# Kernel optimization log

Hardware: AMD Instinct MI355X
Metric: run time of the kernel (lower is better)

Reference implementation:

```python
import jax, jax.numpy as jnp
import numpy as np

EMB = 1024
HEADS = 16
HEAD_DIM = EMB // HEADS


def setup_inputs() -> dict:
    key = jax.random.key(0)
    ks = jax.random.split(key, 12)
    B, S = 4, 2048
    s = 1.0 / np.sqrt(EMB)
    inp = {
        "query": jax.random.normal(ks[0], (B, S, EMB), jnp.float32),
        "key": jax.random.normal(ks[1], (B, S, EMB), jnp.float32),
        "value": jax.random.normal(ks[2], (B, S, EMB), jnp.float32),
        "mask": jax.random.randint(ks[3], (B, 1, 1, S), 0, 2) > 0,
        "Wq": jax.random.normal(ks[4], (EMB, EMB), jnp.float32) * s,
        "bq": jax.random.normal(ks[5], (EMB,), jnp.float32) * s,
        "Wk": jax.random.normal(ks[6], (EMB, EMB), jnp.float32) * s,
        "bk": jax.random.normal(ks[7], (EMB,), jnp.float32) * s,
        "Wv": jax.random.normal(ks[8], (EMB, EMB), jnp.float32) * s,
        "bv": jax.random.normal(ks[9], (EMB,), jnp.float32) * s,
        "Wo": jax.random.normal(ks[10], (EMB, EMB), jnp.float32) * s,
        "bo": jax.random.normal(ks[11], (EMB,), jnp.float32) * s,
    }
    return inp


def _split(x):
    # (B, S, E) -> (B, H, S, D)
    B, S, _ = x.shape
    return x.reshape(B, S, HEADS, HEAD_DIM).transpose(0, 2, 1, 3)


def reference(query, key, value, mask, Wq, bq, Wk, bk, Wv, bv, Wo, bo):
    q = _split(query @ Wq + bq)
    k = _split(key @ Wk + bk)
    v = _split(value @ Wv + bv)
    scale = 1.0 / np.sqrt(HEAD_DIM).astype(np.float32)
    # (B, H, S, S) score matrix, explicitly materialized as in the original
    scores = jnp.einsum("bhqd,bhkd->bhqk", q, k) * scale
    scores = jnp.where(mask, scores, -jnp.inf)
    probs = jax.nn.softmax(scores, axis=-1)
    attn = jnp.einsum("bhqk,bhkd->bhqd", probs, v)
    B, _, S, _ = attn.shape
    out = attn.transpose(0, 2, 1, 3).reshape(B, S, EMB)
    return out @ Wo + bo
```

## Files before the change

### kernel.cpp

```cpp
#include <hip/hip_runtime.h>
#include <hip/hip_bf16.h>
#include <stdint.h>

#define EMB 1024
#define HEADS 16
#define HDIM 64
#define BATCH 4
#define SEQ 2048
#define MTOT (BATCH * SEQ)

typedef unsigned short u16;
typedef __attribute__((ext_vector_type(8))) short bf16x8;
typedef __attribute__((ext_vector_type(4))) float f32x4;

__device__ inline u16 f2bf(float f) {
    uint32_t u = __builtin_bit_cast(uint32_t, f);
    u += 0x7fffu + ((u >> 16) & 1u);
    return (u16)(u >> 16);
}

__device__ inline uint32_t pk2bf(float a, float b) {
    uint32_t ua = __builtin_bit_cast(uint32_t, a) + 0x8000u;
    uint32_t ub = __builtin_bit_cast(uint32_t, b) + 0x8000u;
    return (ua >> 16) | (ub & 0xffff0000u);
}

__device__ inline f32x4 mfma16(bf16x8 a, bf16x8 b, f32x4 c) {
    return __builtin_amdgcn_mfma_f32_16x16x32_bf16(a, b, c, 0, 0, 0);
}

#define GLDS16(gp, lp)                                                        \
    __builtin_amdgcn_global_load_lds(                                         \
        (const __attribute__((address_space(1))) void*)(gp),                  \
        (__attribute__((address_space(3))) void*)(lp), 16, 0, 0)

__global__ void mask_compact(const int* __restrict__ mask,
                             int* __restrict__ cnt, int* __restrict__ idx) {
    __shared__ int ps[256];
    const int b = blockIdx.x, tid = threadIdx.x;
    const int* mp = mask + (size_t)b * SEQ;
    int m[8], s = 0;
#pragma unroll
    for (int e = 0; e < 8; ++e) {
        m[e] = mp[tid * 8 + e] ? 1 : 0;
        s += m[e];
    }
    ps[tid] = s;
    __syncthreads();
    for (int off = 1; off < 256; off <<= 1) {
        int v = (tid >= off) ? ps[tid - off] : 0;
        __syncthreads();
        if (tid >= off) ps[tid] += v;
        __syncthreads();
    }
    const int total = ps[255];
    int r = ps[tid] - s;
#pragma unroll
    for (int e = 0; e < 8; ++e)
        if (m[e]) idx[b * SEQ + r++] = tid * 8 + e;
    if (tid == 0) cnt[b] = total;
}

__global__ void gather_cast(const float* __restrict__ src,
                            const int* __restrict__ idx,
                            const int* __restrict__ cnt,
                            u16* __restrict__ dst) {
    const int row = blockIdx.x;
    const int b = row >> 11, j = row & (SEQ - 1);
    const int cn = cnt[b];
    const int cp = (cn + 127) & ~127;
    if (j >= cp) return;
    const int c4 = threadIdx.x;
    float4 v = {0.f, 0.f, 0.f, 0.f};
    if (j < cn) {
        const int srow = idx[b * SEQ + j];
        v = ((const float4*)(src + (size_t)(b * SEQ + srow) * EMB))[c4];
    }
    ushort4 o;
    o.x = f2bf(v.x); o.y = f2bf(v.y); o.z = f2bf(v.z); o.w = f2bf(v.w);
    ((ushort4*)(dst + (size_t)row * EMB))[c4] = o;
}

__global__ void cast_f32_bf16(const float* __restrict__ src,
                              u16* __restrict__ dst, int n4) {
    int i = blockIdx.x * blockDim.x + threadIdx.x;
    if (i >= n4) return;
    float4 v = ((const float4*)src)[i];
    ushort4 o;
    o.x = f2bf(v.x); o.y = f2bf(v.y); o.z = f2bf(v.z); o.w = f2bf(v.w);
    ((ushort4*)dst)[i] = o;
}

__global__ void transpose_cast(const float* __restrict__ W,
                               u16* __restrict__ Wt) {
    __shared__ u16 T[64][65];
    const int kb = blockIdx.y * 64, nb = blockIdx.x * 64;
    const int tr = threadIdx.x >> 4;
    const int tc = (threadIdx.x & 15) * 4;
#pragma unroll
    for (int j = 0; j < 4; ++j) {
        int r = tr + j * 16;
        float4 v = *(const float4*)&W[(size_t)(kb + r) * EMB + nb + tc];
        T[tc + 0][r] = f2bf(v.x);
        T[tc + 1][r] = f2bf(v.y);
        T[tc + 2][r] = f2bf(v.z);
        T[tc + 3][r] = f2bf(v.w);
    }
    __syncthreads();
#pragma unroll
    for (int j = 0; j < 4; ++j) {
        int rr = tr + j * 16;
        ushort4 o;
        o.x = T[rr][tc]; o.y = T[rr][tc + 1];
        o.z = T[rr][tc + 2]; o.w = T[rr][tc + 3];
        *(ushort4*)&Wt[(size_t)(nb + rr) * EMB + kb + tc] = o;
    }
}

__global__ void transpose_v(const u16* __restrict__ Vp, u16* __restrict__ Vt,
                            const int* __restrict__ cnt) {
    __shared__ u16 T[64][65];
    const int h = blockIdx.x;
    const int b = blockIdx.y >> 5;
    const int s0 = (blockIdx.y & 31) * 64;
    const int cp = (cnt[b] + 127) & ~127;
    if (s0 >= cp) return;
    const int tr = threadIdx.x >> 3;
    const int tc = (threadIdx.x & 7) * 8;
#pragma unroll
    for (int j = 0; j < 2; ++j) {
        int sr = tr + j * 32;
        uint4 v = *(const uint4*)&Vp[(size_t)(b * SEQ + s0 + sr) * EMB +
                                     h * 64 + tc];
        const u16* p = (const u16*)&v;
#pragma unroll
        for (int e = 0; e < 8; ++e) T[tc + e][sr] = p[e];
    }
    __syncthreads();
#pragma unroll
    for (int j = 0; j < 2; ++j) {
        int d = tr + j * 32;
        u16 tmp[8];
#pragma unroll
        for (int e = 0; e < 8; ++e) tmp[e] = T[d][tc + e];
        const int base32 = s0 + (tc & 32);
        const int p0 = ((tc & 8) << 1) + ((tc & 16) >> 2);
        const size_t rowoff =
            ((size_t)(b * HEADS + h) * HDIM + d) * SEQ;
        *(uint2*)&Vt[rowoff + base32 + p0] = *(const uint2*)&tmp[0];
        *(uint2*)&Vt[rowoff + base32 + p0 + 8] = *(const uint2*)&tmp[4];
    }
}

template <bool OUT_BF16>
__global__ __launch_bounds__(256, 2) void gemm_bt(
    const u16* __restrict__ A, const u16* __restrict__ Bt,
    const float* __restrict__ bias, void* __restrict__ C,
    int M, int N, int K, float scale, const int* __restrict__ cnt) {
    __shared__ __align__(16) u16 As[128 * 32];
    __shared__ __align__(16) u16 Bs[128 * 32];
    const int m0 = blockIdx.y * 128, n0 = blockIdx.x * 128;
    if (cnt) {
        const int bb = m0 >> 11;
        const int cp = (cnt[bb] + 127) & ~127;
        if ((m0 & (SEQ - 1)) >= cp) return;
    }
    const int tid = threadIdx.x;
    const int w = tid >> 6, l = tid & 63;
    const int quad = l >> 4, l16 = l & 15;
    const int wm = (w >> 1) * 64, wn = (w & 1) * 64;

    f32x4 acc[4][4];
#pragma unroll
    for (int i = 0; i < 4; ++i)
#pragma unroll
        for (int j = 0; j < 4; ++j) acc[i][j] = (f32x4){0.f, 0.f, 0.f, 0.f};

    for (int k0 = 0; k0 < K; k0 += 32) {
        __syncthreads();
#pragma unroll
        for (int i = 0; i < 2; ++i) {
            int c = (w * 2 + i) * 64 + l;
            int r = c >> 2;
            int sc = (c & 3) ^ ((r >> 1) & 3);
            GLDS16(A + (size_t)(m0 + r) * K + k0 + sc * 8, &As[c * 8]);
            GLDS16(Bt + (size_t)(n0 + r) * K + k0 + sc * 8, &Bs[c * 8]);
        }
        __syncthreads();
        bf16x8 af[4], bfr[4];
#pragma unroll
        for (int mt = 0; mt < 4; ++mt) {
            int ra = wm + mt * 16 + l16;
            af[mt] = *(const bf16x8*)&As[ra * 32 +
                                         ((quad ^ ((ra >> 1) & 3)) * 8)];
        }
#pragma unroll
        for (int nt = 0; nt < 4; ++nt) {
            int rb = wn + nt * 16 + l16;
            bfr[nt] = *(const bf16x8*)&Bs[rb * 32 +
                                          ((quad ^ ((rb >> 1) & 3)) * 8)];
        }
#pragma unroll
        for (int mt = 0; mt < 4; ++mt)
#pragma unroll
            for (int nt = 0; nt < 4; ++nt)
                acc[mt][nt] = mfma16(af[mt], bfr[nt], acc[mt][nt]);
    }

#pragma unroll
    for (int mt = 0; mt < 4; ++mt) {
#pragma unroll
        for (int nt = 0; nt < 4; ++nt) {
            int col = n0 + wn + nt * 16 + l16;
            float bv = bias[col];
#pragma unroll
            for (int r = 0; r < 4; ++r) {
                int row = m0 + wm + mt * 16 + quad * 4 + r;
                float v = (acc[mt][nt][r] + bv) * scale;
                if (OUT_BF16)
                    ((u16*)C)[(size_t)row * N + col] = f2bf(v);
                else
                    ((float*)C)[(size_t)row * N + col] = v;
            }
        }
    }
}

__global__ __launch_bounds__(256, 2) void attn_kernel(
    const u16* __restrict__ Qp, const u16* __restrict__ Kp,
    const u16* __restrict__ Vt, const int* __restrict__ cnt,
    u16* __restrict__ attnb) {
    __shared__ __align__(16) u16 Ks[2][128 * 64];
    __shared__ __align__(16) u16 Vts[2][64 * 128];

    const int tid = threadIdx.x;
    const int w = tid >> 6, l = tid & 63;
    const int quad = l >> 4, l16 = l & 15;

    const int nqb = SEQ / 128;
    const int qb = blockIdx.x % nqb;
    const int bh = blockIdx.x / nqb;
    const int b = bh / HEADS, h = bh % HEADS;
    const int q0 = qb * 128;
    const size_t head_off = (size_t)b * SEQ * EMB + (size_t)h * HDIM;
    const size_t vt_off = (size_t)bh * HDIM * SEQ;

    const int cn = cnt[b];
    const int ntile = ((cn + 127) & ~127) >> 7;

    auto stageKV = [&](int buf, int t) {
#pragma unroll
        for (int i = 0; i < 4; ++i) {
            int c = (w * 4 + i) * 64 + l;
            int r = c >> 3;
            int sc = (c & 7) ^ (r & 7);
            GLDS16(Kp + head_off + (size_t)(t * 128 + r) * EMB + sc * 8,
                   &Ks[buf][c * 8]);
        }
#pragma unroll
        for (int i = 0; i < 4; ++i) {
            int c = (w * 4 + i) * 64 + l;
            int r = c >> 4;
            int sc = (c & 15) ^ (r & 15);
            GLDS16(Vt + vt_off + (size_t)r * SEQ + t * 128 + sc * 8,
                   &Vts[buf][c * 8]);
        }
    };

    bf16x8 bq[2][2];
#pragma unroll
    for (int g = 0; g < 2; ++g) {
        const u16* qrow =
            Qp + head_off + (size_t)(q0 + w * 32 + g * 16 + l16) * EMB;
        bq[g][0] = *(const bf16x8*)(qrow + quad * 8);
        bq[g][1] = *(const bf16x8*)(qrow + 32 + quad * 8);
    }

    bf16x8 ones;
#pragma unroll
    for (int e = 0; e < 8; ++e) ones[e] = (short)0x3f80;

    stageKV(0, 0);
    __syncthreads();

    f32x4 OA[4], OB[4];
#pragma unroll
    for (int i = 0; i < 4; ++i) {
        OA[i] = (f32x4){0.f, 0.f, 0.f, 0.f};
        OB[i] = (f32x4){0.f, 0.f, 0.f, 0.f};
    }
    f32x4 LA = (f32x4){0.f, 0.f, 0.f, 0.f};
    f32x4 LB = (f32x4){0.f, 0.f, 0.f, 0.f};

    auto tilebody = [&](int t, bool last) {
        const int cur = t & 1;
        if (!last) stageKV(cur ^ 1, t + 1);
        const u16* ksb = Ks[cur];
        const u16* vsb = Vts[cur];

        uint32_t pk[2][8][2];
#pragma unroll
        for (int nt = 0; nt < 8; ++nt) {
            int rk = nt * 16 + l16;
            bf16x8 ka0 =
                *(const bf16x8*)&ksb[rk * 64 + ((quad ^ (rk & 7)) * 8)];
            bf16x8 ka1 =
                *(const bf16x8*)&ksb[rk * 64 + (((quad + 4) ^ (rk & 7)) * 8)];
#pragma unroll
            for (int g = 0; g < 2; ++g) {
                f32x4 s = (f32x4){0.f, 0.f, 0.f, 0.f};
                s = mfma16(ka0, bq[g][0], s);
                s = mfma16(ka1, bq[g][1], s);
                f32x4 p;
                if (last) {
                    const int kb = t * 128 + nt * 16 + quad * 4;
#pragma unroll
                    for (int r = 0; r < 4; ++r)
                        p[r] = __builtin_amdgcn_exp2f(
                            (kb + r < cn) ? s[r] : -30000.f);
                } else {
#pragma unroll
                    for (int r = 0; r < 4; ++r)
                        p[r] = __builtin_amdgcn_exp2f(s[r]);
                }
                pk[g][nt][0] = pk2bf(p[0], p[1]);
                pk[g][nt][1] = pk2bf(p[2], p[3]);
            }
        }

#pragma unroll
        for (int i = 0; i < 4; ++i) {
            union { bf16x8 v; uint32_t u[4]; } bpA, bpB;
            bpA.u[0] = pk[0][2 * i][0];
            bpA.u[1] = pk[0][2 * i][1];
            bpA.u[2] = pk[0][2 * i + 1][0];
            bpA.u[3] = pk[0][2 * i + 1][1];
            bpB.u[0] = pk[1][2 * i][0];
            bpB.u[1] = pk[1][2 * i][1];
            bpB.u[2] = pk[1][2 * i + 1][0];
            bpB.u[3] = pk[1][2 * i + 1][1];
            LA = mfma16(ones, bpA.v, LA);
            LB = mfma16(ones, bpB.v, LB);
#pragma unroll
            for (int dt = 0; dt < 4; ++dt) {
                int vd = dt * 16 + l16;
                bf16x8 ap = *(const bf16x8*)&vsb[vd * 128 +
                                                 (((4 * i + quad) ^ (vd & 15)) *
                                                  8)];
                OA[dt] = mfma16(ap, bpA.v, OA[dt]);
                OB[dt] = mfma16(ap, bpB.v, OB[dt]);
            }
        }

        __syncthreads();
    };

    for (int t = 0; t < ntile - 1; ++t) tilebody(t, false);
    tilebody(ntile - 1, true);

#pragma unroll
    for (int g = 0; g < 2; ++g) {
        float inv = 1.0f / (g == 0 ? LA[0] : LB[0]);
        const f32x4* O = (g == 0) ? OA : OB;
        const int orow = q0 + w * 32 + g * 16 + l16;
#pragma unroll
        for (int dt = 0; dt < 4; ++dt) {
            ushort4 o;
            o.x = f2bf(O[dt][0] * inv);
            o.y = f2bf(O[dt][1] * inv);
            o.z = f2bf(O[dt][2] * inv);
            o.w = f2bf(O[dt][3] * inv);
            *(uint2*)&attnb[head_off + (size_t)orow * EMB + dt * 16 +
                            quad * 4] = *(uint2*)&o;
        }
    }
}

extern "C" void kernel_launch(void* const* d_in, const int* in_sizes, int n_in,
                              void* d_out, int out_size, void* d_ws,
                              size_t ws_size, hipStream_t stream) {
    const float* query = (const float*)d_in[0];
    const float* key = (const float*)d_in[1];
    const float* value = (const float*)d_in[2];
    const int* mask = (const int*)d_in[3];
    const float* Wq = (const float*)d_in[4];
    const float* bq = (const float*)d_in[5];
    const float* Wk = (const float*)d_in[6];
    const float* bk = (const float*)d_in[7];
    const float* Wv = (const float*)d_in[8];
    const float* bv = (const float*)d_in[9];
    const float* Wo = (const float*)d_in[10];
    const float* bo = (const float*)d_in[11];

    char* ws = (char*)d_ws;
    const size_t MB = 1ull << 20;
    u16* xq = (u16*)(ws + 0 * MB);
    u16* xk = (u16*)(ws + 16 * MB);
    u16* xv = (u16*)(ws + 32 * MB);
    u16* Wqt = (u16*)(ws + 48 * MB);
    u16* Wkt = (u16*)(ws + 50 * MB);
    u16* Wvt = (u16*)(ws + 52 * MB);
    u16* Wot = (u16*)(ws + 54 * MB);
    u16* Qp = (u16*)(ws + 56 * MB);
    u16* Kp = (u16*)(ws + 72 * MB);
    u16* Vp = (u16*)(ws + 88 * MB);
    u16* attnb = (u16*)(ws + 104 * MB);
    u16* Vt = xq;

    int* cnt = (int*)d_out;
    int* idx = (int*)d_out + 64;

    mask_compact<<<BATCH, 256, 0, stream>>>(mask, cnt, idx);

    const int n4 = MTOT * EMB / 4;
    cast_f32_bf16<<<(n4 + 255) / 256, 256, 0, stream>>>(query, xq, n4);
    gather_cast<<<MTOT, 256, 0, stream>>>(key, idx, cnt, xk);
    gather_cast<<<MTOT, 256, 0, stream>>>(value, idx, cnt, xv);

    dim3 tgrid(EMB / 64, EMB / 64);
    transpose_cast<<<tgrid, 256, 0, stream>>>(Wq, Wqt);
    transpose_cast<<<tgrid, 256, 0, stream>>>(Wk, Wkt);
    transpose_cast<<<tgrid, 256, 0, stream>>>(Wv, Wvt);
    transpose_cast<<<tgrid, 256, 0, stream>>>(Wo, Wot);

    const float c2 = 0.125f * 1.44269504f;
    dim3 ggrid(EMB / 128, MTOT / 128);
    gemm_bt<true><<<ggrid, 256, 0, stream>>>(xq, Wqt, bq, Qp, MTOT, EMB, EMB,
                                             c2, nullptr);
    gemm_bt<true><<<ggrid, 256, 0, stream>>>(xk, Wkt, bk, Kp, MTOT, EMB, EMB,
                                             1.0f, cnt);
    gemm_bt<true><<<ggrid, 256, 0, stream>>>(xv, Wvt, bv, Vp, MTOT, EMB, EMB,
                                             1.0f, cnt);

    transpose_v<<<dim3(HEADS, MTOT / 64), 256, 0, stream>>>(Vp, Vt, cnt);

    attn_kernel<<<BATCH * HEADS * (SEQ / 128), 256, 0, stream>>>(Qp, Kp, Vt,
                                                                 cnt, attnb);

    gemm_bt<false><<<ggrid, 256, 0, stream>>>(attnb, Wot, bo, d_out, MTOT, EMB,
                                              EMB, 1.0f, nullptr);
}
```

Before: 341.0 us.

## Read V directly from global memory and drop its LDS staging buffers

The attention kernel no longer stages the transposed V tiles in double-buffered shared memory. Each wave now loads its V fragments straight from global memory (through the cache) during the PV MFMA loop. Launch bounds rise to 4 blocks per CU, and the probability bf16 packing switches from truncation-style rounding to the HIP round-to-nearest intrinsic. The aim is lower LDS footprint and higher occupancy, at the cost of exposed global-load latency and redundant V reads across waves.

```diff
diff --git a/kernel.cpp b/kernel.cpp
--- a/kernel.cpp
+++ b/kernel.cpp
@@ -19,10 +19,11 @@
     return (u16)(u >> 16);
 }
 
-__device__ inline uint32_t pk2bf(float a, float b) {
-    uint32_t ua = __builtin_bit_cast(uint32_t, a) + 0x8000u;
-    uint32_t ub = __builtin_bit_cast(uint32_t, b) + 0x8000u;
-    return (ua >> 16) | (ub & 0xffff0000u);
+__device__ inline uint32_t pkbf(float a, float b) {
+    __hip_bfloat162 h = __float22bfloat162_rn(make_float2(a, b));
+    uint32_t r;
+    __builtin_memcpy(&r, &h, 4);
+    return r;
 }
 
 __device__ inline f32x4 mfma16(bf16x8 a, bf16x8 b, f32x4 c) {
@@ -226,12 +227,11 @@
     }
 }
 
-__global__ __launch_bounds__(256, 2) void attn_kernel(
+__global__ __launch_bounds__(256, 4) void attn_kernel(
     const u16* __restrict__ Qp, const u16* __restrict__ Kp,
     const u16* __restrict__ Vt, const int* __restrict__ cnt,
     u16* __restrict__ attnb) {
     __shared__ __align__(16) u16 Ks[2][128 * 64];
-    __shared__ __align__(16) u16 Vts[2][64 * 128];
 
     const int tid = threadIdx.x;
     const int w = tid >> 6, l = tid & 63;
@@ -248,7 +248,7 @@
     const int cn = cnt[b];
     const int ntile = ((cn + 127) & ~127) >> 7;
 
-    auto stageKV = [&](int buf, int t) {
+    auto stageK = [&](int buf, int t) {
 #pragma unroll
         for (int i = 0; i < 4; ++i) {
             int c = (w * 4 + i) * 64 + l;
@@ -257,14 +257,6 @@
             GLDS16(Kp + head_off + (size_t)(t * 128 + r) * EMB + sc * 8,
                    &Ks[buf][c * 8]);
         }
-#pragma unroll
-        for (int i = 0; i < 4; ++i) {
-            int c = (w * 4 + i) * 64 + l;
-            int r = c >> 4;
-            int sc = (c & 15) ^ (r & 15);
-            GLDS16(Vt + vt_off + (size_t)r * SEQ + t * 128 + sc * 8,
-                   &Vts[buf][c * 8]);
-        }
     };
 
     bf16x8 bq[2][2];
@@ -280,7 +272,7 @@
 #pragma unroll
     for (int e = 0; e < 8; ++e) ones[e] = (short)0x3f80;
 
-    stageKV(0, 0);
+    stageK(0, 0);
     __syncthreads();
 
     f32x4 OA[4], OB[4];
@@ -294,9 +286,9 @@
 
     auto tilebody = [&](int t, bool last) {
         const int cur = t & 1;
-        if (!last) stageKV(cur ^ 1, t + 1);
+        if (!last) stageK(cur ^ 1, t + 1);
         const u16* ksb = Ks[cur];
-        const u16* vsb = Vts[cur];
+        const u16* vtg = Vt + vt_off + t * 128;
 
         uint32_t pk[2][8][2];
 #pragma unroll
@@ -323,8 +315,8 @@
                     for (int r = 0; r < 4; ++r)
                         p[r] = __builtin_amdgcn_exp2f(s[r]);
                 }
-                pk[g][nt][0] = pk2bf(p[0], p[1]);
-                pk[g][nt][1] = pk2bf(p[2], p[3]);
+                pk[g][nt][0] = pkbf(p[0], p[1]);
+                pk[g][nt][1] = pkbf(p[2], p[3]);
             }
         }
 
@@ -344,9 +336,8 @@
 #pragma unroll
             for (int dt = 0; dt < 4; ++dt) {
                 int vd = dt * 16 + l16;
-                bf16x8 ap = *(const bf16x8*)&vsb[vd * 128 +
-                                                 (((4 * i + quad) ^ (vd & 15)) *
-                                                  8)];
+                bf16x8 ap = *(const bf16x8*)&vtg[(size_t)vd * SEQ +
+                                                 (4 * i + quad) * 8];
                 OA[dt] = mfma16(ap, bpA.v, OA[dt]);
                 OB[dt] = mfma16(ap, bpB.v, OB[dt]);
             }
```

Result: slower. 449.3 us (+31.8%).

## Double-buffer GEMM LDS tiles and use intrinsic bf16 pair conversion

Applied to the files above, without the earlier changes.

The projection GEMM now keeps two LDS buffers and issues the global-to-LDS loads for the next K slice before computing on the current one, with one barrier per iteration instead of two. This is meant to hide global load latency behind the MFMA work, at the cost of doubling the LDS used by the GEMM, which may reduce occupancy. The attention kernel's probability packing switches from a manual round-half-up bit trick to the library float2-to-bfloat162 round-to-nearest-even conversion, which may map to a hardware pack instruction.

```diff
diff --git a/kernel.cpp b/kernel.cpp
--- a/kernel.cpp
+++ b/kernel.cpp
@@ -19,10 +19,11 @@
     return (u16)(u >> 16);
 }
 
-__device__ inline uint32_t pk2bf(float a, float b) {
-    uint32_t ua = __builtin_bit_cast(uint32_t, a) + 0x8000u;
-    uint32_t ub = __builtin_bit_cast(uint32_t, b) + 0x8000u;
-    return (ua >> 16) | (ub & 0xffff0000u);
+__device__ inline uint32_t pkbf(float a, float b) {
+    __hip_bfloat162 h = __float22bfloat162_rn(make_float2(a, b));
+    uint32_t r;
+    __builtin_memcpy(&r, &h, 4);
+    return r;
 }
 
 __device__ inline f32x4 mfma16(bf16x8 a, bf16x8 b, f32x4 c) {
@@ -157,8 +158,8 @@
     const u16* __restrict__ A, const u16* __restrict__ Bt,
     const float* __restrict__ bias, void* __restrict__ C,
     int M, int N, int K, float scale, const int* __restrict__ cnt) {
-    __shared__ __align__(16) u16 As[128 * 32];
-    __shared__ __align__(16) u16 Bs[128 * 32];
+    __shared__ __align__(16) u16 As[2][128 * 32];
+    __shared__ __align__(16) u16 Bs[2][128 * 32];
     const int m0 = blockIdx.y * 128, n0 = blockIdx.x * 128;
     if (cnt) {
         const int bb = m0 >> 11;
@@ -170,41 +171,48 @@
     const int quad = l >> 4, l16 = l & 15;
     const int wm = (w >> 1) * 64, wn = (w & 1) * 64;
 
-    f32x4 acc[4][4];
-#pragma unroll
-    for (int i = 0; i < 4; ++i)
-#pragma unroll
-        for (int j = 0; j < 4; ++j) acc[i][j] = (f32x4){0.f, 0.f, 0.f, 0.f};
-
-    for (int k0 = 0; k0 < K; k0 += 32) {
-        __syncthreads();
+    auto stage = [&](int buf, int k0) {
 #pragma unroll
         for (int i = 0; i < 2; ++i) {
             int c = (w * 2 + i) * 64 + l;
             int r = c >> 2;
             int sc = (c & 3) ^ ((r >> 1) & 3);
-            GLDS16(A + (size_t)(m0 + r) * K + k0 + sc * 8, &As[c * 8]);
-            GLDS16(Bt + (size_t)(n0 + r) * K + k0 + sc * 8, &Bs[c * 8]);
-        }
-        __syncthreads();
+            GLDS16(A + (size_t)(m0 + r) * K + k0 + sc * 8, &As[buf][c * 8]);
+            GLDS16(Bt + (size_t)(n0 + r) * K + k0 + sc * 8, &Bs[buf][c * 8]);
+        }
+    };
+
+    f32x4 acc[4][4];
+#pragma unroll
+    for (int i = 0; i < 4; ++i)
+#pragma unroll
+        for (int j = 0; j < 4; ++j) acc[i][j] = (f32x4){0.f, 0.f, 0.f, 0.f};
+
+    stage(0, 0);
+    __syncthreads();
+
+    int cur = 0;
+    for (int k0 = 0; k0 < K; k0 += 32, cur ^= 1) {
+        if (k0 + 32 < K) stage(cur ^ 1, k0 + 32);
         bf16x8 af[4], bfr[4];
 #pragma unroll
         for (int mt = 0; mt < 4; ++mt) {
             int ra = wm + mt * 16 + l16;
-            af[mt] = *(const bf16x8*)&As[ra * 32 +
-                                         ((quad ^ ((ra >> 1) & 3)) * 8)];
+            af[mt] = *(const bf16x8*)&As[cur][ra * 32 +
+                                             ((quad ^ ((ra >> 1) & 3)) * 8)];
         }
 #pragma unroll
         for (int nt = 0; nt < 4; ++nt) {
             int rb = wn + nt * 16 + l16;
-            bfr[nt] = *(const bf16x8*)&Bs[rb * 32 +
-                                          ((quad ^ ((rb >> 1) & 3)) * 8)];
+            bfr[nt] = *(const bf16x8*)&Bs[cur][rb * 32 +
+                                              ((quad ^ ((rb >> 1) & 3)) * 8)];
         }
 #pragma unroll
         for (int mt = 0; mt < 4; ++mt)
 #pragma unroll
             for (int nt = 0; nt < 4; ++nt)
                 acc[mt][nt] = mfma16(af[mt], bfr[nt], acc[mt][nt]);
+        __syncthreads();
     }
 
 #pragma unroll
@@ -323,8 +331,8 @@
                     for (int r = 0; r < 4; ++r)
                         p[r] = __builtin_amdgcn_exp2f(s[r]);
                 }
-                pk[g][nt][0] = pk2bf(p[0], p[1]);
-                pk[g][nt][1] = pk2bf(p[2], p[3]);
+                pk[g][nt][0] = pkbf(p[0], p[1]);
+                pk[g][nt][1] = pkbf(p[2], p[3]);
             }
         }
 
```

Measured after the change: 342.0 us. No clear change (+0.3%).
